# Kernel optimization log

Measured on AMD Instinct MI355X. Metric: run time of the kernel, lower is better.

## Reference

```python
import jax, jax.numpy as jnp
import numpy as np

B, S, C = 16384, 64, 9      # batch, seq_len, input_channels (3x3 rotation, flattened)
H, BN = 128, 64             # hidden_channels, bottle_neck_channel


def setup_inputs() -> dict:
    key = jax.random.key(0)
    ks = jax.random.split(key, 12)
    t = jnp.broadcast_to(jnp.linspace(0.0, 1.0, S, dtype=jnp.float32)[None, :], (B, S))
    x = jax.random.normal(ks[0], (B, S, C), dtype=jnp.float32)
    s = lambda fi, fo: 1.0 / np.sqrt(fi)
    return {
        "t": t, "x": x,
        # CDEFunc MLP params (hidden -> bottleneck -> bottleneck -> bottleneck -> hidden*input)
        "W1": jax.random.normal(ks[1], (H, BN), jnp.float32) * s(H, BN),  "b1": jnp.zeros((BN,), jnp.float32),
        "W2": jax.random.normal(ks[2], (BN, BN), jnp.float32) * s(BN, BN), "b2": jnp.zeros((BN,), jnp.float32),
        "W3": jax.random.normal(ks[3], (BN, BN), jnp.float32) * s(BN, BN), "b3": jnp.zeros((BN,), jnp.float32),
        "W4": jax.random.normal(ks[4], (BN, H * C), jnp.float32) * s(BN, H * C), "b4": jnp.zeros((H * C,), jnp.float32),
        # initial map input -> hidden, readout hidden -> output (9D)
        "Wi": jax.random.normal(ks[5], (C, H), jnp.float32) * s(C, H), "bi": jnp.zeros((H,), jnp.float32),
        "Wo": jax.random.normal(ks[6], (H, C), jnp.float32) * s(H, C), "bo": jnp.zeros((C,), jnp.float32),
    }


def _cde_field(z, W1, b1, W2, b2, W3, b3, W4, b4):
    """f(t,z): (B,H) -> (B,H,C). 4-layer MLP, elu/elu/elu/tanh, as in CDEFunc."""
    h = jax.nn.elu(z @ W1 + b1)
    h = jax.nn.elu(h @ W2 + b2)
    h = jax.nn.elu(h @ W3 + b3)
    h = jnp.tanh(h @ W4 + b4)
    return h.reshape(z.shape[:-1] + (H, C))


def reference(t, x, W1, b1, W2, b2, W3, b3, W4, b4, Wi, bi, Wo, bo):
    # Linear interpolation of the control path X: dX/dt is constant on each knot
    # interval, matching LinearInterpolation (SO3 paths drop the time channel,
    # so the control derivative has C channels).
    t1d = t[0]                                   # (S,) shared time grid
    dt = t1d[1:] - t1d[:-1]                      # (S-1,)
    dX = (x[:, 1:] - x[:, :-1]) / dt[None, :, None]  # (B, S-1, C)

    z0 = x[:, 0] @ Wi + bi                       # initial hidden state (B, H)

    def g(z, dXk):
        # dz/dt = f(t,z) @ dX/dt  -> (B,H)
        f = _cde_field(z, W1, b1, W2, b2, W3, b3, W4, b4)
        return jnp.einsum("bhc,bc->bh", f, dXk)

    def rk4_step(z, inp):
        dXk, h = inp                             # h: interval length (scalar)
        k1 = g(z, dXk)
        k2 = g(z + 0.5 * h * k1, dXk)
        k3 = g(z + 0.5 * h * k2, dXk)
        k4 = g(z + h * k3, dXk)
        z = z + (h / 6.0) * (k1 + 2.0 * k2 + 2.0 * k3 + k4)
        return z, None

    dX_t = jnp.transpose(dX, (1, 0, 2))          # (S-1, B, C) for scan
    zT, _ = jax.lax.scan(rk4_step, z0, (dX_t, dt))
    return zT @ Wo + bo                          # (B, output_channel)
```

## Files before the change

kernel.cpp:

```cpp
#include <hip/hip_runtime.h>
#include <cstdint>
#include <cstddef>


typedef _Float16 f16;
typedef _Float16 f16x8 __attribute__((ext_vector_type(8)));
typedef float f32x4 __attribute__((ext_vector_type(4)));

#define LOG2E     1.44269504088896340736f
#define TWOLOG2E  2.88539008177792681472f

#define MFMA3(acc, ah, al, bh, bl)                                        \
  acc = __builtin_amdgcn_mfma_f32_16x16x32_f16(ah, bh, acc, 0, 0, 0);     \
  acc = __builtin_amdgcn_mfma_f32_16x16x32_f16(al, bh, acc, 0, 0, 0);     \
  acc = __builtin_amdgcn_mfma_f32_16x16x32_f16(ah, bl, acc, 0, 0, 0);

__global__ void pack_weights(const float* __restrict__ W1, const float* __restrict__ W2,
                             const float* __restrict__ W3, const float* __restrict__ W4,
                             f16* __restrict__ wp)
{
  int t = blockIdx.x * 256 + threadIdx.x;
  if (t >= 90112) return;
  float v;
  if (t < 8192) {
    int j = t & 7, lr = (t >> 3) & 63, kb = (t >> 9) & 3, nt = t >> 11;
    int k = 32*kb + 8*(lr >> 4) + j, n = 16*nt + (lr & 15);
    v = W1[k*64 + n];
  } else if (t < 12288) {
    int u = t - 8192;
    int j = u & 7, lr = (u >> 3) & 63, kb = (u >> 9) & 1, nt = u >> 10;
    int k = 32*kb + 8*(lr >> 4) + j, n = 16*nt + (lr & 15);
    v = W2[k*64 + n];
  } else if (t < 16384) {
    int u = t - 12288;
    int j = u & 7, lr = (u >> 3) & 63, kb = (u >> 9) & 1, nt = u >> 10;
    int k = 32*kb + 8*(lr >> 4) + j, n = 16*nt + (lr & 15);
    v = W3[k*64 + n];
  } else {
    int u = t - 16384;
    int j = u & 7, lr = (u >> 3) & 63, kb = (u >> 9) & 1, nt = (u >> 10) & 7, c = u >> 13;
    int k = 32*kb + 8*(lr >> 4) + j, h = 16*nt + (lr & 15);
    v = W4[k*1152 + 9*h + c];
  }
  f16 hi = (f16)v;
  wp[t] = hi;
  wp[90112 + t] = (f16)(v - (float)hi);
}

__global__ __launch_bounds__(512, 2) void cde_main(
    const float* __restrict__ x, const f16* __restrict__ wp,
    const float* __restrict__ b1, const float* __restrict__ b2,
    const float* __restrict__ b3, const float* __restrict__ b4,
    const float* __restrict__ Wi, const float* __restrict__ bi,
    const float* __restrict__ Wo, const float* __restrict__ bo,
    float* __restrict__ out)
{
  constexpr int SH = 0, SL = 16384, HAH = 32768, HAL = 40960, HBH = 49152, HBL = 57344;
  constexpr int UT = 65536, WH = 67840, WL = 100608, B4S = 133376;
  __shared__ __attribute__((aligned(16))) char smem[137984];

  const int tid = threadIdx.x;
  const int w   = tid >> 6;
  const int l   = tid & 63;
  const int l15 = l & 15, l4 = l >> 4;
  const int mh  = w >> 2, nq = w & 3;
  const int b0  = blockIdx.x << 6;
  const int colG4 = (w << 4) + l15;
  const int xorv  = (l15 & 7) << 4;

  const f16x8* wpv = reinterpret_cast<const f16x8*>(wp);
  const f16x8* wlv = wpv + 11264;

  const float b1v = b1[(nq<<4) + l15], b2v = b2[(nq<<4) + l15], b3v = b3[(nq<<4) + l15];
  const float b1x = b1v * LOG2E, b2x = b2v * LOG2E, b3x = b3v * LOG2E;

  const f32x4 zero4 = {0.f, 0.f, 0.f, 0.f};

  {
    const f32x4* wp4 = reinterpret_cast<const f32x4*>(wp);
    for (int idx = tid; idx < 2048; idx += 512) {
      ((f32x4*)(smem + WH))[idx] = wp4[idx];
      ((f32x4*)(smem + WL))[idx] = wp4[11264 + idx];
    }
  }
  for (int idx = tid; idx < 1152; idx += 512) {
    int h = idx / 9, c = idx - h*9;
    ((float*)(smem + B4S))[c*128 + h] = b4[idx] * TWOLOG2E;
  }
  for (int idx = tid; idx < 1152; idx += 512) ((float*)(smem + HAH))[idx] = Wi[idx];
  for (int idx = tid; idx <  128; idx += 512) ((float*)(smem + HBH))[idx] = bi[idx];
  for (int idx = tid; idx <  576; idx += 512) {
    int row = idx / 9, c = idx - row*9;
    ((float*)(smem + UT))[c*64 + row] = x[(size_t)(b0 + row)*576 + c];
  }
  __syncthreads();

  f32x4 z[4], ark[4];
  {
    float wiv[9];
#pragma unroll
    for (int c = 0; c < 9; c++) wiv[c] = ((const float*)(smem + HAH))[c*128 + colG4];
    float biv = ((const float*)(smem + HBH))[colG4];
#pragma unroll
    for (int mi = 0; mi < 4; mi++) {
      f32x4 zz = {biv, biv, biv, biv};
#pragma unroll
      for (int c = 0; c < 9; c++) {
        f32x4 xv = *reinterpret_cast<const f32x4*>(smem + UT + c*256 + mi*64 + l4*16);
#pragma unroll
        for (int r = 0; r < 4; r++) zz[r] = __builtin_fmaf(xv[r], wiv[c], zz[r]);
      }
      z[mi] = zz;
#pragma unroll
      for (int r = 0; r < 4; r++) {
        int row  = 16*mi + 4*l4 + r;
        int byte = row*256 + ((colG4*2) ^ ((row & 7) << 4));
        f16 hi = (f16)zz[r];
        *reinterpret_cast<f16*>(smem + SH + byte) = hi;
        *reinterpret_cast<f16*>(smem + SL + byte) = (f16)(zz[r] - (float)hi);
      }
    }
  }

#pragma unroll 1
  for (int k = 0; k < 63; ++k) {
    __syncthreads();
    {
      const float* xk = x + (size_t)b0*576 + (size_t)k*9;
      for (int idx = tid; idx < 576; idx += 512) {
        int row = idx / 9, c = idx - row*9;
        const float* p = xk + (size_t)row*576 + c;
        ((float*)(smem + UT))[c*64 + row] = p[9] - p[0];
      }
    }
#pragma unroll 1
    for (int st = 0; st < 4; ++st) {
      __syncthreads();

      {
        f32x4 acc[2];
        acc[0] = zero4; acc[1] = zero4;
#pragma unroll
        for (int kb = 0; kb < 4; kb++) {
          int wb = ((nq*4 + kb)*64 + l)*16;
          f16x8 bh = *reinterpret_cast<const f16x8*>(smem + WH + wb);
          f16x8 bl = *reinterpret_cast<const f16x8*>(smem + WL + wb);
#pragma unroll
          for (int mi = 0; mi < 2; mi++) {
            int row = 32*mh + 16*mi + l15;
            int off = row*256 + ((16*l4 + 64*kb) ^ xorv);
            f16x8 ah = *reinterpret_cast<const f16x8*>(smem + SH + off);
            f16x8 al = *reinterpret_cast<const f16x8*>(smem + SL + off);
            MFMA3(acc[mi], ah, al, bh, bl);
          }
        }
#pragma unroll
        for (int mi = 0; mi < 2; mi++)
#pragma unroll
          for (int r = 0; r < 4; r++) {
            float pre = acc[mi][r];
            float lin = pre + b1v;
            float e   = __builtin_amdgcn_exp2f(__builtin_fmaf(pre, LOG2E, b1x)) - 1.0f;
            float res = lin > 0.0f ? lin : e;
            int row  = 32*mh + 16*mi + 4*l4 + r;
            int byte = row*128 + ((((nq<<4) + l15)*2) ^ ((row & 7) << 4));
            f16 hi = (f16)res;
            *reinterpret_cast<f16*>(smem + HAH + byte) = hi;
            *reinterpret_cast<f16*>(smem + HAL + byte) = (f16)(res - (float)hi);
          }
      }
      __syncthreads();

      {
        f32x4 acc[2];
        acc[0] = zero4; acc[1] = zero4;
#pragma unroll
        for (int kb = 0; kb < 2; kb++) {
          int wb = (1024 + (nq*2 + kb)*64 + l)*16;
          f16x8 bh = *reinterpret_cast<const f16x8*>(smem + WH + wb);
          f16x8 bl = *reinterpret_cast<const f16x8*>(smem + WL + wb);
#pragma unroll
          for (int mi = 0; mi < 2; mi++) {
            int row = 32*mh + 16*mi + l15;
            int off = row*128 + ((16*l4 + 64*kb) ^ xorv);
            f16x8 ah = *reinterpret_cast<const f16x8*>(smem + HAH + off);
            f16x8 al = *reinterpret_cast<const f16x8*>(smem + HAL + off);
            MFMA3(acc[mi], ah, al, bh, bl);
          }
        }
#pragma unroll
        for (int mi = 0; mi < 2; mi++)
#pragma unroll
          for (int r = 0; r < 4; r++) {
            float pre = acc[mi][r];
            float lin = pre + b2v;
            float e   = __builtin_amdgcn_exp2f(__builtin_fmaf(pre, LOG2E, b2x)) - 1.0f;
            float res = lin > 0.0f ? lin : e;
            int row  = 32*mh + 16*mi + 4*l4 + r;
            int byte = row*128 + ((((nq<<4) + l15)*2) ^ ((row & 7) << 4));
            f16 hi = (f16)res;
            *reinterpret_cast<f16*>(smem + HBH + byte) = hi;
            *reinterpret_cast<f16*>(smem + HBL + byte) = (f16)(res - (float)hi);
          }
      }
      __syncthreads();

      {
        f32x4 acc[2];
        acc[0] = zero4; acc[1] = zero4;
#pragma unroll
        for (int kb = 0; kb < 2; kb++) {
          int wb = (1536 + (nq*2 + kb)*64 + l)*16;
          f16x8 bh = *reinterpret_cast<const f16x8*>(smem + WH + wb);
          f16x8 bl = *reinterpret_cast<const f16x8*>(smem + WL + wb);
#pragma unroll
          for (int mi = 0; mi < 2; mi++) {
            int row = 32*mh + 16*mi + l15;
            int off = row*128 + ((16*l4 + 64*kb) ^ xorv);
            f16x8 ah = *reinterpret_cast<const f16x8*>(smem + HBH + off);
            f16x8 al = *reinterpret_cast<const f16x8*>(smem + HBL + off);
            MFMA3(acc[mi], ah, al, bh, bl);
          }
        }
#pragma unroll
        for (int mi = 0; mi < 2; mi++)
#pragma unroll
          for (int r = 0; r < 4; r++) {
            float pre = acc[mi][r];
            float lin = pre + b3v;
            float e   = __builtin_amdgcn_exp2f(__builtin_fmaf(pre, LOG2E, b3x)) - 1.0f;
            float res = lin > 0.0f ? lin : e;
            int row  = 32*mh + 16*mi + 4*l4 + r;
            int byte = row*128 + ((((nq<<4) + l15)*2) ^ ((row & 7) << 4));
            f16 hi = (f16)res;
            *reinterpret_cast<f16*>(smem + HAH + byte) = hi;
            *reinterpret_cast<f16*>(smem + HAL + byte) = (f16)(res - (float)hi);
          }
      }
      __syncthreads();

      {
        f16x8 a4h[4][2], a4l[4][2];
#pragma unroll
        for (int mi = 0; mi < 4; mi++)
#pragma unroll
          for (int kb = 0; kb < 2; kb++) {
            int row = 16*mi + l15;
            int off = row*128 + ((16*l4 + 64*kb) ^ xorv);
            a4h[mi][kb] = *reinterpret_cast<const f16x8*>(smem + HAH + off);
            a4l[mi][kb] = *reinterpret_cast<const f16x8*>(smem + HAL + off);
          }
        f32x4 K4[4];
#pragma unroll
        for (int mi = 0; mi < 4; mi++) K4[mi] = zero4;

        int ib = 2048 + (w*2)*64 + l;
        f16x8 cbh0 = wpv[ib], cbl0 = wlv[ib], cbh1 = wpv[ib + 64], cbl1 = wlv[ib + 64];
#pragma unroll 1
        for (int c = 0; c < 9; c++) {
          f16x8 bh0 = cbh0, bl0 = cbl0, bh1 = cbh1, bl1 = cbl1;
          if (c < 8) {
            int jb = 2048 + (((c + 1)*8 + w)*2)*64 + l;
            cbh0 = wpv[jb]; cbl0 = wlv[jb]; cbh1 = wpv[jb + 64]; cbl1 = wlv[jb + 64];
          }
          f32x4 ac[4];
#pragma unroll
          for (int mi = 0; mi < 4; mi++) {
            ac[mi] = zero4;
            MFMA3(ac[mi], a4h[mi][0], a4l[mi][0], bh0, bl0);
            MFMA3(ac[mi], a4h[mi][1], a4l[mi][1], bh1, bl1);
          }
          float b4c = ((const float*)(smem + B4S))[c*128 + colG4];
#pragma unroll
          for (int mi = 0; mi < 4; mi++) {
            f32x4 uv = *reinterpret_cast<const f32x4*>(smem + UT + c*256 + mi*64 + l4*16);
#pragma unroll
            for (int r = 0; r < 4; r++) {
              float tex = __builtin_amdgcn_exp2f(__builtin_fmaf(ac[mi][r], TWOLOG2E, b4c));
              float th  = __builtin_fmaf(__builtin_amdgcn_rcpf(tex + 1.0f), -2.0f, 1.0f);
              K4[mi][r] = __builtin_fmaf(th, uv[r], K4[mi][r]);
            }
          }
        }
        if (st == 0) {
#pragma unroll
          for (int mi = 0; mi < 4; mi++) ark[mi] = K4[mi];
        } else if (st == 3) {
#pragma unroll
          for (int mi = 0; mi < 4; mi++)
#pragma unroll
            for (int r = 0; r < 4; r++)
              z[mi][r] = __builtin_fmaf(ark[mi][r] + K4[mi][r], 0.166666666667f, z[mi][r]);
        } else {
#pragma unroll
          for (int mi = 0; mi < 4; mi++)
#pragma unroll
            for (int r = 0; r < 4; r++)
              ark[mi][r] = __builtin_fmaf(2.0f, K4[mi][r], ark[mi][r]);
        }
        const float alpha = (st == 2) ? 1.0f : 0.5f;
#pragma unroll
        for (int mi = 0; mi < 4; mi++)
#pragma unroll
          for (int r = 0; r < 4; r++) {
            float sv = (st == 3) ? z[mi][r] : __builtin_fmaf(alpha, K4[mi][r], z[mi][r]);
            int row  = 16*mi + 4*l4 + r;
            int byte = row*256 + ((colG4*2) ^ ((row & 7) << 4));
            f16 hi = (f16)sv;
            *reinterpret_cast<f16*>(smem + SH + byte) = hi;
            *reinterpret_cast<f16*>(smem + SL + byte) = (f16)(sv - (float)hi);
          }
      }
    }
  }

  __syncthreads();
#pragma unroll
  for (int mi = 0; mi < 4; mi++)
#pragma unroll
    for (int r = 0; r < 4; r++) {
      int row = 16*mi + 4*l4 + r;
      ((float*)smem)[row*128 + colG4] = z[mi][r];
    }
  for (int idx = tid; idx < 1152; idx += 512) ((float*)(smem + HBH))[idx] = Wo[idx];
  __syncthreads();
  for (int idx = tid; idx < 576; idx += 512) {
    int b_ = idx / 9, c = idx - b_*9;
    float acc = bo[c];
#pragma unroll 4
    for (int h = 0; h < 128; h++)
      acc = __builtin_fmaf(((const float*)smem)[b_*128 + h],
                           ((const float*)(smem + HBH))[h*9 + c], acc);
    out[(size_t)(b0 + b_)*9 + c] = acc;
  }
}

extern "C" void kernel_launch(void* const* d_in, const int* in_sizes, int n_in,
                              void* d_out, int out_size, void* d_ws, size_t ws_size,
                              hipStream_t stream)
{
  const float* x  = (const float*)d_in[1];
  const float* W1 = (const float*)d_in[2];
  const float* b1 = (const float*)d_in[3];
  const float* W2 = (const float*)d_in[4];
  const float* b2 = (const float*)d_in[5];
  const float* W3 = (const float*)d_in[6];
  const float* b3 = (const float*)d_in[7];
  const float* W4 = (const float*)d_in[8];
  const float* b4 = (const float*)d_in[9];
  const float* Wi = (const float*)d_in[10];
  const float* bi = (const float*)d_in[11];
  const float* Wo = (const float*)d_in[12];
  const float* bo = (const float*)d_in[13];
  f16* wp = (f16*)d_ws;

  pack_weights<<<352, 256, 0, stream>>>(W1, W2, W3, W4, wp);
  cde_main<<<256, 512, 0, stream>>>(x, wp, b1, b2, b3, b4, Wi, bi, Wo, bo, (float*)d_out);
}
```

Measured before the change: 2.758 ms.

## Double threads per block to 1024 and halve per-wave row tiles

Raises each block from 8 to 16 waves. Each wave now handles 16 rows in layers 1-3, and 32 rows with one column group in the W4 layer, instead of twice that. This adds latency-hiding parallelism per CU, since there are only 256 blocks with large LDS each. In exchange, every barrier now synchronises twice as many waves, and each wave has less MFMA work to amortise its weight loads. The launch bound of 1024 with a minimum of 4 also tightens the register budget.

```diff
diff --git a/kernel.cpp b/kernel.cpp
--- a/kernel.cpp
+++ b/kernel.cpp
@@ -47,7 +47,7 @@
   wp[90112 + t] = (f16)(v - (float)hi);
 }
 
-__global__ __launch_bounds__(512, 2) void cde_main(
+__global__ __launch_bounds__(1024, 4) void cde_main(
     const float* __restrict__ x, const f16* __restrict__ wp,
     const float* __restrict__ b1, const float* __restrict__ b2,
     const float* __restrict__ b3, const float* __restrict__ b4,
@@ -64,8 +64,9 @@
   const int l   = tid & 63;
   const int l15 = l & 15, l4 = l >> 4;
   const int mh  = w >> 2, nq = w & 3;
+  const int mg  = w >> 3, cg = w & 7;
   const int b0  = blockIdx.x << 6;
-  const int colG4 = (w << 4) + l15;
+  const int colG4 = (cg << 4) + l15;
   const int xorv  = (l15 & 7) << 4;
 
   const f16x8* wpv = reinterpret_cast<const f16x8*>(wp);
@@ -78,42 +79,42 @@
 
   {
     const f32x4* wp4 = reinterpret_cast<const f32x4*>(wp);
-    for (int idx = tid; idx < 2048; idx += 512) {
+    for (int idx = tid; idx < 2048; idx += 1024) {
       ((f32x4*)(smem + WH))[idx] = wp4[idx];
       ((f32x4*)(smem + WL))[idx] = wp4[11264 + idx];
     }
   }
-  for (int idx = tid; idx < 1152; idx += 512) {
+  for (int idx = tid; idx < 1152; idx += 1024) {
     int h = idx / 9, c = idx - h*9;
     ((float*)(smem + B4S))[c*128 + h] = b4[idx] * TWOLOG2E;
   }
-  for (int idx = tid; idx < 1152; idx += 512) ((float*)(smem + HAH))[idx] = Wi[idx];
-  for (int idx = tid; idx <  128; idx += 512) ((float*)(smem + HBH))[idx] = bi[idx];
-  for (int idx = tid; idx <  576; idx += 512) {
-    int row = idx / 9, c = idx - row*9;
+  for (int idx = tid; idx < 1152; idx += 1024) ((float*)(smem + HAH))[idx] = Wi[idx];
+  if (tid < 128) ((float*)(smem + HBH))[tid] = bi[tid];
+  if (tid < 576) {
+    int row = tid / 9, c = tid - row*9;
     ((float*)(smem + UT))[c*64 + row] = x[(size_t)(b0 + row)*576 + c];
   }
   __syncthreads();
 
-  f32x4 z[4], ark[4];
+  f32x4 z[2], ark[2];
   {
     float wiv[9];
 #pragma unroll
     for (int c = 0; c < 9; c++) wiv[c] = ((const float*)(smem + HAH))[c*128 + colG4];
     float biv = ((const float*)(smem + HBH))[colG4];
 #pragma unroll
-    for (int mi = 0; mi < 4; mi++) {
+    for (int mi = 0; mi < 2; mi++) {
       f32x4 zz = {biv, biv, biv, biv};
 #pragma unroll
       for (int c = 0; c < 9; c++) {
-        f32x4 xv = *reinterpret_cast<const f32x4*>(smem + UT + c*256 + mi*64 + l4*16);
+        f32x4 xv = *reinterpret_cast<const f32x4*>(smem + UT + c*256 + 128*mg + 64*mi + 16*l4);
 #pragma unroll
         for (int r = 0; r < 4; r++) zz[r] = __builtin_fmaf(xv[r], wiv[c], zz[r]);
       }
       z[mi] = zz;
 #pragma unroll
       for (int r = 0; r < 4; r++) {
-        int row  = 16*mi + 4*l4 + r;
+        int row  = 32*mg + 16*mi + 4*l4 + r;
         int byte = row*256 + ((colG4*2) ^ ((row & 7) << 4));
         f16 hi = (f16)zz[r];
         *reinterpret_cast<f16*>(smem + SH + byte) = hi;
@@ -125,155 +126,133 @@
 #pragma unroll 1
   for (int k = 0; k < 63; ++k) {
     __syncthreads();
-    {
-      const float* xk = x + (size_t)b0*576 + (size_t)k*9;
-      for (int idx = tid; idx < 576; idx += 512) {
-        int row = idx / 9, c = idx - row*9;
-        const float* p = xk + (size_t)row*576 + c;
-        ((float*)(smem + UT))[c*64 + row] = p[9] - p[0];
-      }
+    if (tid < 576) {
+      int row = tid / 9, c = tid - row*9;
+      const float* p = x + (size_t)(b0 + row)*576 + (size_t)k*9 + c;
+      ((float*)(smem + UT))[c*64 + row] = p[9] - p[0];
     }
 #pragma unroll 1
     for (int st = 0; st < 4; ++st) {
       __syncthreads();
 
       {
-        f32x4 acc[2];
-        acc[0] = zero4; acc[1] = zero4;
+        f32x4 acc = zero4;
 #pragma unroll
         for (int kb = 0; kb < 4; kb++) {
           int wb = ((nq*4 + kb)*64 + l)*16;
           f16x8 bh = *reinterpret_cast<const f16x8*>(smem + WH + wb);
           f16x8 bl = *reinterpret_cast<const f16x8*>(smem + WL + wb);
-#pragma unroll
-          for (int mi = 0; mi < 2; mi++) {
-            int row = 32*mh + 16*mi + l15;
-            int off = row*256 + ((16*l4 + 64*kb) ^ xorv);
-            f16x8 ah = *reinterpret_cast<const f16x8*>(smem + SH + off);
-            f16x8 al = *reinterpret_cast<const f16x8*>(smem + SL + off);
-            MFMA3(acc[mi], ah, al, bh, bl);
-          }
-        }
-#pragma unroll
-        for (int mi = 0; mi < 2; mi++)
-#pragma unroll
-          for (int r = 0; r < 4; r++) {
-            float pre = acc[mi][r];
-            float lin = pre + b1v;
-            float e   = __builtin_amdgcn_exp2f(__builtin_fmaf(pre, LOG2E, b1x)) - 1.0f;
-            float res = lin > 0.0f ? lin : e;
-            int row  = 32*mh + 16*mi + 4*l4 + r;
-            int byte = row*128 + ((((nq<<4) + l15)*2) ^ ((row & 7) << 4));
-            f16 hi = (f16)res;
-            *reinterpret_cast<f16*>(smem + HAH + byte) = hi;
-            *reinterpret_cast<f16*>(smem + HAL + byte) = (f16)(res - (float)hi);
-          }
+          int row = 16*mh + l15;
+          int off = row*256 + ((16*l4 + 64*kb) ^ xorv);
+          f16x8 ah = *reinterpret_cast<const f16x8*>(smem + SH + off);
+          f16x8 al = *reinterpret_cast<const f16x8*>(smem + SL + off);
+          MFMA3(acc, ah, al, bh, bl);
+        }
+#pragma unroll
+        for (int r = 0; r < 4; r++) {
+          float pre = acc[r];
+          float lin = pre + b1v;
+          float e   = __builtin_amdgcn_exp2f(__builtin_fmaf(pre, LOG2E, b1x)) - 1.0f;
+          float res = lin > 0.0f ? lin : e;
+          int row  = 16*mh + 4*l4 + r;
+          int byte = row*128 + ((((nq<<4) + l15)*2) ^ ((row & 7) << 4));
+          f16 hi = (f16)res;
+          *reinterpret_cast<f16*>(smem + HAH + byte) = hi;
+          *reinterpret_cast<f16*>(smem + HAL + byte) = (f16)(res - (float)hi);
+        }
       }
       __syncthreads();
 
       {
-        f32x4 acc[2];
-        acc[0] = zero4; acc[1] = zero4;
+        f32x4 acc = zero4;
 #pragma unroll
         for (int kb = 0; kb < 2; kb++) {
           int wb = (1024 + (nq*2 + kb)*64 + l)*16;
           f16x8 bh = *reinterpret_cast<const f16x8*>(smem + WH + wb);
           f16x8 bl = *reinterpret_cast<const f16x8*>(smem + WL + wb);
-#pragma unroll
-          for (int mi = 0; mi < 2; mi++) {
-            int row = 32*mh + 16*mi + l15;
-            int off = row*128 + ((16*l4 + 64*kb) ^ xorv);
-            f16x8 ah = *reinterpret_cast<const f16x8*>(smem + HAH + off);
-            f16x8 al = *reinterpret_cast<const f16x8*>(smem + HAL + off);
-            MFMA3(acc[mi], ah, al, bh, bl);
-          }
-        }
-#pragma unroll
-        for (int mi = 0; mi < 2; mi++)
-#pragma unroll
-          for (int r = 0; r < 4; r++) {
-            float pre = acc[mi][r];
-            float lin = pre + b2v;
-            float e   = __builtin_amdgcn_exp2f(__builtin_fmaf(pre, LOG2E, b2x)) - 1.0f;
-            float res = lin > 0.0f ? lin : e;
-            int row  = 32*mh + 16*mi + 4*l4 + r;
-            int byte = row*128 + ((((nq<<4) + l15)*2) ^ ((row & 7) << 4));
-            f16 hi = (f16)res;
-            *reinterpret_cast<f16*>(smem + HBH + byte) = hi;
-            *reinterpret_cast<f16*>(smem + HBL + byte) = (f16)(res - (float)hi);
-          }
+          int row = 16*mh + l15;
+          int off = row*128 + ((16*l4 + 64*kb) ^ xorv);
+          f16x8 ah = *reinterpret_cast<const f16x8*>(smem + HAH + off);
+          f16x8 al = *reinterpret_cast<const f16x8*>(smem + HAL + off);
+          MFMA3(acc, ah, al, bh, bl);
+        }
+#pragma unroll
+        for (int r = 0; r < 4; r++) {
+          float pre = acc[r];
+          float lin = pre + b2v;
+          float e   = __builtin_amdgcn_exp2f(__builtin_fmaf(pre, LOG2E, b2x)) - 1.0f;
+          float res = lin > 0.0f ? lin : e;
+          int row  = 16*mh + 4*l4 + r;
+          int byte = row*128 + ((((nq<<4) + l15)*2) ^ ((row & 7) << 4));
+          f16 hi = (f16)res;
+          *reinterpret_cast<f16*>(smem + HBH + byte) = hi;
+          *reinterpret_cast<f16*>(smem + HBL + byte) = (f16)(res - (float)hi);
+        }
       }
       __syncthreads();
 
       {
-        f32x4 acc[2];
-        acc[0] = zero4; acc[1] = zero4;
+        f32x4 acc = zero4;
 #pragma unroll
         for (int kb = 0; kb < 2; kb++) {
           int wb = (1536 + (nq*2 + kb)*64 + l)*16;
           f16x8 bh = *reinterpret_cast<const f16x8*>(smem + WH + wb);
           f16x8 bl = *reinterpret_cast<const f16x8*>(smem + WL + wb);
-#pragma unroll
-          for (int mi = 0; mi < 2; mi++) {
-            int row = 32*mh + 16*mi + l15;
-            int off = row*128 + ((16*l4 + 64*kb) ^ xorv);
-            f16x8 ah = *reinterpret_cast<const f16x8*>(smem + HBH + off);
-            f16x8 al = *reinterpret_cast<const f16x8*>(smem + HBL + off);
-            MFMA3(acc[mi], ah, al, bh, bl);
-          }
-        }
+          int row = 16*mh + l15;
+          int off = row*128 + ((16*l4 + 64*kb) ^ xorv);
+          f16x8 ah = *reinterpret_cast<const f16x8*>(smem + HBH + off);
+          f16x8 al = *reinterpret_cast<const f16x8*>(smem + HBL + off);
+          MFMA3(acc, ah, al, bh, bl);
+        }
+#pragma unroll
+        for (int r = 0; r < 4; r++) {
+          float pre = acc[r];
+          float lin = pre + b3v;
+          float e   = __builtin_amdgcn_exp2f(__builtin_fmaf(pre, LOG2E, b3x)) - 1.0f;
+          float res = lin > 0.0f ? lin : e;
+          int row  = 16*mh + 4*l4 + r;
+          int byte = row*128 + ((((nq<<4) + l15)*2) ^ ((row & 7) << 4));
+          f16 hi = (f16)res;
+          *reinterpret_cast<f16*>(smem + HAH + byte) = hi;
+          *reinterpret_cast<f16*>(smem + HAL + byte) = (f16)(res - (float)hi);
+        }
+      }
+      __syncthreads();
+
+      {
+        f16x8 a4h[2][2], a4l[2][2];
 #pragma unroll
         for (int mi = 0; mi < 2; mi++)
 #pragma unroll
-          for (int r = 0; r < 4; r++) {
-            float pre = acc[mi][r];
-            float lin = pre + b3v;
-            float e   = __builtin_amdgcn_exp2f(__builtin_fmaf(pre, LOG2E, b3x)) - 1.0f;
-            float res = lin > 0.0f ? lin : e;
-            int row  = 32*mh + 16*mi + 4*l4 + r;
-            int byte = row*128 + ((((nq<<4) + l15)*2) ^ ((row & 7) << 4));
-            f16 hi = (f16)res;
-            *reinterpret_cast<f16*>(smem + HAH + byte) = hi;
-            *reinterpret_cast<f16*>(smem + HAL + byte) = (f16)(res - (float)hi);
-          }
-      }
-      __syncthreads();
-
-      {
-        f16x8 a4h[4][2], a4l[4][2];
-#pragma unroll
-        for (int mi = 0; mi < 4; mi++)
-#pragma unroll
           for (int kb = 0; kb < 2; kb++) {
-            int row = 16*mi + l15;
+            int row = 32*mg + 16*mi + l15;
             int off = row*128 + ((16*l4 + 64*kb) ^ xorv);
             a4h[mi][kb] = *reinterpret_cast<const f16x8*>(smem + HAH + off);
             a4l[mi][kb] = *reinterpret_cast<const f16x8*>(smem + HAL + off);
           }
-        f32x4 K4[4];
-#pragma unroll
-        for (int mi = 0; mi < 4; mi++) K4[mi] = zero4;
-
-        int ib = 2048 + (w*2)*64 + l;
+        f32x4 K4[2];
+        K4[0] = zero4; K4[1] = zero4;
+
+        int ib = 2048 + (cg*2)*64 + l;
         f16x8 cbh0 = wpv[ib], cbl0 = wlv[ib], cbh1 = wpv[ib + 64], cbl1 = wlv[ib + 64];
 #pragma unroll 1
         for (int c = 0; c < 9; c++) {
           f16x8 bh0 = cbh0, bl0 = cbl0, bh1 = cbh1, bl1 = cbl1;
           if (c < 8) {
-            int jb = 2048 + (((c + 1)*8 + w)*2)*64 + l;
+            int jb = 2048 + (((c + 1)*8 + cg)*2)*64 + l;
             cbh0 = wpv[jb]; cbl0 = wlv[jb]; cbh1 = wpv[jb + 64]; cbl1 = wlv[jb + 64];
           }
-          f32x4 ac[4];
-#pragma unroll
-          for (int mi = 0; mi < 4; mi++) {
+          f32x4 ac[2];
+#pragma unroll
+          for (int mi = 0; mi < 2; mi++) {
             ac[mi] = zero4;
             MFMA3(ac[mi], a4h[mi][0], a4l[mi][0], bh0, bl0);
             MFMA3(ac[mi], a4h[mi][1], a4l[mi][1], bh1, bl1);
           }
           float b4c = ((const float*)(smem + B4S))[c*128 + colG4];
 #pragma unroll
-          for (int mi = 0; mi < 4; mi++) {
-            f32x4 uv = *reinterpret_cast<const f32x4*>(smem + UT + c*256 + mi*64 + l4*16);
+          for (int mi = 0; mi < 2; mi++) {
+            f32x4 uv = *reinterpret_cast<const f32x4*>(smem + UT + c*256 + 128*mg + 64*mi + 16*l4);
 #pragma unroll
             for (int r = 0; r < 4; r++) {
               float tex = __builtin_amdgcn_exp2f(__builtin_fmaf(ac[mi][r], TWOLOG2E, b4c));
@@ -284,27 +263,27 @@
         }
         if (st == 0) {
 #pragma unroll
-          for (int mi = 0; mi < 4; mi++) ark[mi] = K4[mi];
+          for (int mi = 0; mi < 2; mi++) ark[mi] = K4[mi];
         } else if (st == 3) {
 #pragma unroll
-          for (int mi = 0; mi < 4; mi++)
+          for (int mi = 0; mi < 2; mi++)
 #pragma unroll
             for (int r = 0; r < 4; r++)
               z[mi][r] = __builtin_fmaf(ark[mi][r] + K4[mi][r], 0.166666666667f, z[mi][r]);
         } else {
 #pragma unroll
-          for (int mi = 0; mi < 4; mi++)
+          for (int mi = 0; mi < 2; mi++)
 #pragma unroll
             for (int r = 0; r < 4; r++)
               ark[mi][r] = __builtin_fmaf(2.0f, K4[mi][r], ark[mi][r]);
         }
         const float alpha = (st == 2) ? 1.0f : 0.5f;
 #pragma unroll
-        for (int mi = 0; mi < 4; mi++)
+        for (int mi = 0; mi < 2; mi++)
 #pragma unroll
           for (int r = 0; r < 4; r++) {
             float sv = (st == 3) ? z[mi][r] : __builtin_fmaf(alpha, K4[mi][r], z[mi][r]);
-            int row  = 16*mi + 4*l4 + r;
+            int row  = 32*mg + 16*mi + 4*l4 + r;
             int byte = row*256 + ((colG4*2) ^ ((row & 7) << 4));
             f16 hi = (f16)sv;
             *reinterpret_cast<f16*>(smem + SH + byte) = hi;
@@ -316,16 +295,16 @@
 
   __syncthreads();
 #pragma unroll
-  for (int mi = 0; mi < 4; mi++)
+  for (int mi = 0; mi < 2; mi++)
 #pragma unroll
     for (int r = 0; r < 4; r++) {
-      int row = 16*mi + 4*l4 + r;
+      int row = 32*mg + 16*mi + 4*l4 + r;
       ((float*)smem)[row*128 + colG4] = z[mi][r];
     }
-  for (int idx = tid; idx < 1152; idx += 512) ((float*)(smem + HBH))[idx] = Wo[idx];
+  for (int idx = tid; idx < 1152; idx += 1024) ((float*)(smem + HBH))[idx] = Wo[idx];
   __syncthreads();
-  for (int idx = tid; idx < 576; idx += 512) {
-    int b_ = idx / 9, c = idx - b_*9;
+  if (tid < 576) {
+    int b_ = tid / 9, c = tid - b_*9;
     float acc = bo[c];
 #pragma unroll 4
     for (int h = 0; h < 128; h++)
@@ -355,5 +334,5 @@
   f16* wp = (f16*)d_ws;
 
   pack_weights<<<352, 256, 0, stream>>>(W1, W2, W3, W4, wp);
-  cde_main<<<256, 512, 0, stream>>>(x, wp, b1, b2, b3, b4, Wi, bi, Wo, bo, (float*)d_out);
+  cde_main<<<256, 1024, 0, stream>>>(x, wp, b1, b2, b3, b4, Wi, bi, Wo, bo, (float*)d_out);
 }
```

Result: slower. 3.191 ms (+15.7%).

## Retile W4 GEMM into 2x2 warp tiles with double-buffered weight prefetch

Applied to the files above, without the earlier changes.

Changes the last-layer work split from each warp owning 16 hidden columns across all 64 rows to a 32-row by 32-column tile per warp. This halves the A-fragment loads per warp, but each warp now fetches twice as many B weights per channel. The 9-channel loop is software-pipelined with two register sets (A/B) that prefetch the next channel's W4 fragments from global memory. The first set is loaded at stage start, overlapping the earlier layers, and the per-step dX load is folded into stage 0, removing one barrier per step. Register pressure rises (16 f16x8 weight registers live), which could hurt occupancy under launch_bounds(512,2).

```diff
diff --git a/kernel.cpp b/kernel.cpp
--- a/kernel.cpp
+++ b/kernel.cpp
@@ -47,6 +47,43 @@
   wp[90112 + t] = (f16)(v - (float)hi);
 }
 
+__device__ __forceinline__ void tanh_k4(f32x4& K, const f32x4 ac, float b4c, const f32x4 uv) {
+#pragma unroll
+  for (int r = 0; r < 4; r++) {
+    float tex = __builtin_amdgcn_exp2f(__builtin_fmaf(ac[r], TWOLOG2E, b4c));
+    float th  = __builtin_fmaf(__builtin_amdgcn_rcpf(tex + 1.0f), -2.0f, 1.0f);
+    K[r] = __builtin_fmaf(th, uv[r], K[r]);
+  }
+}
+
+#define LOADSET(P, c) do {                                                \
+    int base_ = 2048 + (((c)*8 + 2*nq)*2)*64 + l;                         \
+    P##h00 = wpv[base_];       P##l00 = wlv[base_];                       \
+    P##h01 = wpv[base_ + 64];  P##l01 = wlv[base_ + 64];                  \
+    P##h10 = wpv[base_ + 128]; P##l10 = wlv[base_ + 128];                 \
+    P##h11 = wpv[base_ + 192]; P##l11 = wlv[base_ + 192];                 \
+  } while (0)
+
+#define COMPUTE(P, c) do {                                                \
+    f32x4 ac00 = zero4, ac01 = zero4, ac10 = zero4, ac11 = zero4;         \
+    MFMA3(ac00, a4h[0][0], a4l[0][0], P##h00, P##l00);                    \
+    MFMA3(ac00, a4h[0][1], a4l[0][1], P##h01, P##l01);                    \
+    MFMA3(ac01, a4h[0][0], a4l[0][0], P##h10, P##l10);                    \
+    MFMA3(ac01, a4h[0][1], a4l[0][1], P##h11, P##l11);                    \
+    MFMA3(ac10, a4h[1][0], a4l[1][0], P##h00, P##l00);                    \
+    MFMA3(ac10, a4h[1][1], a4l[1][1], P##h01, P##l01);                    \
+    MFMA3(ac11, a4h[1][0], a4l[1][0], P##h10, P##l10);                    \
+    MFMA3(ac11, a4h[1][1], a4l[1][1], P##h11, P##l11);                    \
+    float b4c0 = ((const float*)(smem + B4S))[(c)*128 + 32*nq + l15];     \
+    float b4c1 = ((const float*)(smem + B4S))[(c)*128 + 32*nq + 16 + l15];\
+    f32x4 uv0 = *reinterpret_cast<const f32x4*>(smem + UT + (c)*256 + 128*mh + 16*l4);      \
+    f32x4 uv1 = *reinterpret_cast<const f32x4*>(smem + UT + (c)*256 + 128*mh + 64 + 16*l4); \
+    tanh_k4(K4[0][0], ac00, b4c0, uv0);                                   \
+    tanh_k4(K4[0][1], ac01, b4c1, uv0);                                   \
+    tanh_k4(K4[1][0], ac10, b4c0, uv1);                                   \
+    tanh_k4(K4[1][1], ac11, b4c1, uv1);                                   \
+  } while (0)
+
 __global__ __launch_bounds__(512, 2) void cde_main(
     const float* __restrict__ x, const f16* __restrict__ wp,
     const float* __restrict__ b1, const float* __restrict__ b2,
@@ -65,7 +102,6 @@
   const int l15 = l & 15, l4 = l >> 4;
   const int mh  = w >> 2, nq = w & 3;
   const int b0  = blockIdx.x << 6;
-  const int colG4 = (w << 4) + l15;
   const int xorv  = (l15 & 7) << 4;
 
   const f16x8* wpv = reinterpret_cast<const f16x8*>(wp);
@@ -95,47 +131,62 @@
   }
   __syncthreads();
 
-  f32x4 z[4], ark[4];
+  f32x4 z[2][2], ark[2][2], K4[2][2];
   {
-    float wiv[9];
-#pragma unroll
-    for (int c = 0; c < 9; c++) wiv[c] = ((const float*)(smem + HAH))[c*128 + colG4];
-    float biv = ((const float*)(smem + HBH))[colG4];
-#pragma unroll
-    for (int mi = 0; mi < 4; mi++) {
-      f32x4 zz = {biv, biv, biv, biv};
+    float wiv0[9], wiv1[9];
+#pragma unroll
+    for (int c = 0; c < 9; c++) {
+      wiv0[c] = ((const float*)(smem + HAH))[c*128 + 32*nq + l15];
+      wiv1[c] = ((const float*)(smem + HAH))[c*128 + 32*nq + 16 + l15];
+    }
+    float biv0 = ((const float*)(smem + HBH))[32*nq + l15];
+    float biv1 = ((const float*)(smem + HBH))[32*nq + 16 + l15];
+#pragma unroll
+    for (int mi = 0; mi < 2; mi++) {
+      f32x4 zz0 = {biv0, biv0, biv0, biv0};
+      f32x4 zz1 = {biv1, biv1, biv1, biv1};
 #pragma unroll
       for (int c = 0; c < 9; c++) {
-        f32x4 xv = *reinterpret_cast<const f32x4*>(smem + UT + c*256 + mi*64 + l4*16);
-#pragma unroll
-        for (int r = 0; r < 4; r++) zz[r] = __builtin_fmaf(xv[r], wiv[c], zz[r]);
-      }
-      z[mi] = zz;
-#pragma unroll
-      for (int r = 0; r < 4; r++) {
-        int row  = 16*mi + 4*l4 + r;
-        int byte = row*256 + ((colG4*2) ^ ((row & 7) << 4));
-        f16 hi = (f16)zz[r];
-        *reinterpret_cast<f16*>(smem + SH + byte) = hi;
-        *reinterpret_cast<f16*>(smem + SL + byte) = (f16)(zz[r] - (float)hi);
-      }
+        f32x4 xv = *reinterpret_cast<const f32x4*>(smem + UT + c*256 + 128*mh + 64*mi + 16*l4);
+#pragma unroll
+        for (int r = 0; r < 4; r++) {
+          zz0[r] = __builtin_fmaf(xv[r], wiv0[c], zz0[r]);
+          zz1[r] = __builtin_fmaf(xv[r], wiv1[c], zz1[r]);
+        }
+      }
+      z[mi][0] = zz0; z[mi][1] = zz1;
+#pragma unroll
+      for (int ng = 0; ng < 2; ng++)
+#pragma unroll
+        for (int r = 0; r < 4; r++) {
+          int row  = 32*mh + 16*mi + 4*l4 + r;
+          int col  = 32*nq + 16*ng + l15;
+          int byte = row*256 + ((col*2) ^ ((row & 7) << 4));
+          float sv = z[mi][ng][r];
+          f16 hi = (f16)sv;
+          *reinterpret_cast<f16*>(smem + SH + byte) = hi;
+          *reinterpret_cast<f16*>(smem + SL + byte) = (f16)(sv - (float)hi);
+        }
     }
   }
 
 #pragma unroll 1
   for (int k = 0; k < 63; ++k) {
-    __syncthreads();
-    {
-      const float* xk = x + (size_t)b0*576 + (size_t)k*9;
-      for (int idx = tid; idx < 576; idx += 512) {
-        int row = idx / 9, c = idx - row*9;
-        const float* p = xk + (size_t)row*576 + c;
-        ((float*)(smem + UT))[c*64 + row] = p[9] - p[0];
-      }
-    }
 #pragma unroll 1
     for (int st = 0; st < 4; ++st) {
       __syncthreads();
+
+      f16x8 Ah00, Ah01, Ah10, Ah11, Al00, Al01, Al10, Al11;
+      f16x8 Bh00, Bh01, Bh10, Bh11, Bl00, Bl01, Bl10, Bl11;
+      LOADSET(A, 0);
+
+      if (st == 0) {
+        for (int idx = tid; idx < 576; idx += 512) {
+          int row = idx / 9, c = idx - row*9;
+          const float* p = x + (size_t)(b0 + row)*576 + (size_t)k*9 + c;
+          ((float*)(smem + UT))[c*64 + row] = p[9] - p[0];
+        }
+      }
 
       {
         f32x4 acc[2];
@@ -240,88 +291,82 @@
       __syncthreads();
 
       {
-        f16x8 a4h[4][2], a4l[4][2];
-#pragma unroll
-        for (int mi = 0; mi < 4; mi++)
+        f16x8 a4h[2][2], a4l[2][2];
+#pragma unroll
+        for (int mi = 0; mi < 2; mi++)
 #pragma unroll
           for (int kb = 0; kb < 2; kb++) {
-            int row = 16*mi + l15;
+            int row = 32*mh + 16*mi + l15;
             int off = row*128 + ((16*l4 + 64*kb) ^ xorv);
             a4h[mi][kb] = *reinterpret_cast<const f16x8*>(smem + HAH + off);
             a4l[mi][kb] = *reinterpret_cast<const f16x8*>(smem + HAL + off);
           }
-        f32x4 K4[4];
-#pragma unroll
-        for (int mi = 0; mi < 4; mi++) K4[mi] = zero4;
-
-        int ib = 2048 + (w*2)*64 + l;
-        f16x8 cbh0 = wpv[ib], cbl0 = wlv[ib], cbh1 = wpv[ib + 64], cbl1 = wlv[ib + 64];
+        K4[0][0] = zero4; K4[0][1] = zero4; K4[1][0] = zero4; K4[1][1] = zero4;
+
+        LOADSET(B, 1);
 #pragma unroll 1
-        for (int c = 0; c < 9; c++) {
-          f16x8 bh0 = cbh0, bl0 = cbl0, bh1 = cbh1, bl1 = cbl1;
-          if (c < 8) {
-            int jb = 2048 + (((c + 1)*8 + w)*2)*64 + l;
-            cbh0 = wpv[jb]; cbl0 = wlv[jb]; cbh1 = wpv[jb + 64]; cbl1 = wlv[jb + 64];
-          }
-          f32x4 ac[4];
-#pragma unroll
-          for (int mi = 0; mi < 4; mi++) {
-            ac[mi] = zero4;
-            MFMA3(ac[mi], a4h[mi][0], a4l[mi][0], bh0, bl0);
-            MFMA3(ac[mi], a4h[mi][1], a4l[mi][1], bh1, bl1);
-          }
-          float b4c = ((const float*)(smem + B4S))[c*128 + colG4];
-#pragma unroll
-          for (int mi = 0; mi < 4; mi++) {
-            f32x4 uv = *reinterpret_cast<const f32x4*>(smem + UT + c*256 + mi*64 + l4*16);
+        for (int cc = 0; cc < 4; ++cc) {
+          COMPUTE(A, 2*cc);
+          LOADSET(A, 2*cc + 2);
+          COMPUTE(B, 2*cc + 1);
+          if (cc < 3) LOADSET(B, 2*cc + 3);
+        }
+        COMPUTE(A, 8);
+
+        if (st == 0) {
+#pragma unroll
+          for (int mi = 0; mi < 2; mi++)
+#pragma unroll
+            for (int ng = 0; ng < 2; ng++) ark[mi][ng] = K4[mi][ng];
+        } else if (st == 3) {
+#pragma unroll
+          for (int mi = 0; mi < 2; mi++)
+#pragma unroll
+            for (int ng = 0; ng < 2; ng++)
+#pragma unroll
+              for (int r = 0; r < 4; r++)
+                z[mi][ng][r] = __builtin_fmaf(ark[mi][ng][r] + K4[mi][ng][r],
+                                              0.166666666667f, z[mi][ng][r]);
+        } else {
+#pragma unroll
+          for (int mi = 0; mi < 2; mi++)
+#pragma unroll
+            for (int ng = 0; ng < 2; ng++)
+#pragma unroll
+              for (int r = 0; r < 4; r++)
+                ark[mi][ng][r] = __builtin_fmaf(2.0f, K4[mi][ng][r], ark[mi][ng][r]);
+        }
+        const float alpha = (st == 2) ? 1.0f : 0.5f;
+#pragma unroll
+        for (int mi = 0; mi < 2; mi++)
+#pragma unroll
+          for (int ng = 0; ng < 2; ng++)
 #pragma unroll
             for (int r = 0; r < 4; r++) {
-              float tex = __builtin_amdgcn_exp2f(__builtin_fmaf(ac[mi][r], TWOLOG2E, b4c));
-              float th  = __builtin_fmaf(__builtin_amdgcn_rcpf(tex + 1.0f), -2.0f, 1.0f);
-              K4[mi][r] = __builtin_fmaf(th, uv[r], K4[mi][r]);
+              float sv = (st == 3) ? z[mi][ng][r]
+                                   : __builtin_fmaf(alpha, K4[mi][ng][r], z[mi][ng][r]);
+              int row  = 32*mh + 16*mi + 4*l4 + r;
+              int col  = 32*nq + 16*ng + l15;
+              int byte = row*256 + ((col*2) ^ ((row & 7) << 4));
+              f16 hi = (f16)sv;
+              *reinterpret_cast<f16*>(smem + SH + byte) = hi;
+              *reinterpret_cast<f16*>(smem + SL + byte) = (f16)(sv - (float)hi);
             }
-          }
-        }
-        if (st == 0) {
-#pragma unroll
-          for (int mi = 0; mi < 4; mi++) ark[mi] = K4[mi];
-        } else if (st == 3) {
-#pragma unroll
-          for (int mi = 0; mi < 4; mi++)
-#pragma unroll
-            for (int r = 0; r < 4; r++)
-              z[mi][r] = __builtin_fmaf(ark[mi][r] + K4[mi][r], 0.166666666667f, z[mi][r]);
-        } else {
-#pragma unroll
-          for (int mi = 0; mi < 4; mi++)
-#pragma unroll
-            for (int r = 0; r < 4; r++)
-              ark[mi][r] = __builtin_fmaf(2.0f, K4[mi][r], ark[mi][r]);
-        }
-        const float alpha = (st == 2) ? 1.0f : 0.5f;
-#pragma unroll
-        for (int mi = 0; mi < 4; mi++)
-#pragma unroll
-          for (int r = 0; r < 4; r++) {
-            float sv = (st == 3) ? z[mi][r] : __builtin_fmaf(alpha, K4[mi][r], z[mi][r]);
-            int row  = 16*mi + 4*l4 + r;
-            int byte = row*256 + ((colG4*2) ^ ((row & 7) << 4));
-            f16 hi = (f16)sv;
-            *reinterpret_cast<f16*>(smem + SH + byte) = hi;
-            *reinterpret_cast<f16*>(smem + SL + byte) = (f16)(sv - (float)hi);
-          }
       }
     }
   }
 
   __syncthreads();
 #pragma unroll
-  for (int mi = 0; mi < 4; mi++)
-#pragma unroll
-    for (int r = 0; r < 4; r++) {
-      int row = 16*mi + 4*l4 + r;
-      ((float*)smem)[row*128 + colG4] = z[mi][r];
-    }
+  for (int mi = 0; mi < 2; mi++)
+#pragma unroll
+    for (int ng = 0; ng < 2; ng++)
+#pragma unroll
+      for (int r = 0; r < 4; r++) {
+        int row = 32*mh + 16*mi + 4*l4 + r;
+        int col = 32*nq + 16*ng + l15;
+        ((float*)smem)[row*128 + col] = z[mi][ng][r];
+      }
   for (int idx = tid; idx < 1152; idx += 512) ((float*)(smem + HBH))[idx] = Wo[idx];
   __syncthreads();
   for (int idx = tid; idx < 576; idx += 512) {
```

Result: slower. 3.478 ms (+26.1%).
